# Performance work log

Hardware: AMD Instinct MI355X
Metric: run time of the kernel (lower is better)

## Reference

```python
import jax, jax.numpy as jnp
import numpy as np

H = 384
W = 384
C_X = 64       # channels of x (== out_channels)
C_PTX = 64     # channels of ptx
C_IN = C_X + C_PTX  # Linear in_channels = 128
C_OUT = 64
N_TGT = 120000  # number of target pixels (CSR segments)
DEG = 8         # points per target pixel
N_PTS = N_TGT * DEG


def setup_inputs() -> dict:
    key = jax.random.key(0)
    k1, k2, k3, k4 = jax.random.split(key, 4)
    x = jax.random.normal(k1, (1, C_X, H, W), jnp.float32)
    ptx = jax.random.normal(k2, (N_PTS, C_PTX), jnp.float32)
    # CSR row pointer over points per target pixel (monotone, ends at N_PTS)
    point_key = jnp.arange(N_TGT + 1, dtype=jnp.int32) * DEG
    # unique target-pixel indices into H*W
    pixel_tgt_idx = jnp.arange(N_TGT, dtype=jnp.int32)
    sm_w = jax.random.normal(k3, (C_IN, 1), jnp.float32) * 0.05
    sm_b = jnp.zeros((1,), jnp.float32)
    fo_w = jax.random.normal(k4, (C_IN, C_OUT), jnp.float32) * 0.05
    fo_b = jnp.zeros((C_OUT,), jnp.float32)
    return {"x": x, "ptx": ptx, "sm_w": sm_w, "sm_b": sm_b,
            "fo_w": fo_w, "fo_b": fo_b, "point_key": point_key,
            "pixel_tgt_idx": pixel_tgt_idx, "bs": 1, "height": H, "width": W}


def reference(x, ptx, sm_w, sm_b, fo_w, fo_b, point_key, pixel_tgt_idx, bs, height, width):
    # segment id per point from CSR rowptr (static total length for jit)
    seg = jnp.repeat(jnp.arange(N_TGT, dtype=jnp.int32), jnp.diff(point_key),
                     total_repeat_length=N_PTS)
    # pixel features gathered to target pixels, then CSR-gathered to points
    feat_px = x.transpose(0, 2, 3, 1).reshape(height * width, C_X)[pixel_tgt_idx]
    feat = jnp.concatenate([ptx, feat_px[seg]], axis=1)  # [N_PTS, C_IN]
    # _net_forward: identity (base class)
    # segment softmax over points within each pixel group
    logits = feat @ sm_w + sm_b  # [N_PTS, 1]
    m = jax.ops.segment_max(logits, seg, num_segments=N_TGT)
    e = jnp.exp(logits - m[seg])
    s = jax.ops.segment_sum(e, seg, num_segments=N_TGT)
    weight = e / (s[seg] + 1e-16)
    # feat_out projection replaces ptx
    ptx_out = feat @ fo_w + fo_b  # [N_PTS, C_OUT]
    agg = jax.ops.segment_sum(weight * ptx_out, seg, num_segments=N_TGT)  # [N_TGT, C_OUT]
    # list_to_map: scatter aggregated features back to image grid + mask
    flat = jnp.zeros((height * width, C_OUT), x.dtype).at[pixel_tgt_idx].set(agg)
    mask = jnp.zeros((height * width, 1), x.dtype).at[pixel_tgt_idx].set(1.0)
    fmap = flat.reshape(1, height, width, C_OUT).transpose(0, 3, 1, 2)
    mmap = mask.reshape(1, height, width, 1).transpose(0, 3, 1, 2)
    x_out = jnp.where(mmap > 0, fmap, x)
    return x_out, ptx_out
```

## Files before the change

### kernel.cpp

```cpp
#include <hip/hip_runtime.h>
#include <hip/hip_bf16.h>
#include <math.h>

typedef __attribute__((ext_vector_type(8))) short short8v;
typedef __attribute__((ext_vector_type(4))) short short4v;
typedef __attribute__((ext_vector_type(4))) float float4v;

#define TB 64

__device__ __forceinline__ short f2bf(float f) {
    __hip_bfloat16 h = __float2bfloat16(f);
    short s; __builtin_memcpy(&s, &h, sizeof(short));
    return s;
}
__device__ __forceinline__ float bf2f(short u) {
    unsigned int x = ((unsigned int)(unsigned short)u) << 16;
    float f; __builtin_memcpy(&f, &x, sizeof(float));
    return f;
}
__device__ __forceinline__ float4v mfma_bf16(short8v a, short8v b, float4v c) {
    return __builtin_amdgcn_mfma_f32_16x16x32_bf16(a, b, c, 0, 0, 0);
}

__device__ __forceinline__ int WTI(int row, int col) {
    return row * 72 + (col ^ (((row >> 2) & 7) << 3));
}

__global__ __launch_bounds__(256)
void mask_set_kernel(const int* __restrict__ idx, unsigned char* __restrict__ mask, int n) {
    int i = blockIdx.x * blockDim.x + threadIdx.x;
    if (i < n) mask[idx[i]] = 1;
}

__global__ __launch_bounds__(256)
void copy_masked_kernel(const float4* __restrict__ x, float4* __restrict__ out,
                        const unsigned int* __restrict__ mask4, int q4n) {
    int q = blockIdx.x * blockDim.x + threadIdx.x;
    if (q >= q4n) return;
    if (mask4[q] == 0x01010101u) return;
    size_t idx = (size_t)blockIdx.y * q4n + q;
    out[idx] = x[idx];
}

__global__ __launch_bounds__(256)
void copy_x_kernel(const float4* __restrict__ x, float4* __restrict__ out, int n4) {
    int i = blockIdx.x * blockDim.x + threadIdx.x;
    if (i < n4) out[i] = x[i];
}

__global__ __launch_bounds__(256, 4)
void fused_kernel(const float* __restrict__ x,
                  const float* __restrict__ ptx,
                  const float* __restrict__ sm_w,
                  const float* __restrict__ fo_w,
                  const float* __restrict__ fo_b,
                  const int* __restrict__ point_key,
                  const int* __restrict__ pixel_tgt_idx,
                  float* __restrict__ xout,
                  float* __restrict__ ptx_out,
                  int n_tgt, int n_pts, int hw)
{
    __shared__ __align__(16) char sraw[27648];
    unsigned short (*fpx)[72]   = (unsigned short (*)[72])sraw;
    unsigned short* wTf         = (unsigned short*)(sraw + 9216);
    unsigned short (*q_lds)[72] = (unsigned short (*)[72])sraw;
    float (*agg)[68]            = (float (*)[68])(sraw + 9216);
    __shared__ int pix_s[TB], r0_s[TB], deg_s[TB];

    const int tid  = threadIdx.x;
    const int lane = tid & 63;
    const int w    = tid >> 6;
    const int lo16 = lane & 15;
    const int g    = lane >> 4;
    const int t0   = blockIdx.x * TB;
    const int tw0  = w * 16;

    float4 wv[8];
    {
        const float4* fw4 = (const float4*)fo_w;
        #pragma unroll
        for (int i = 0; i < 8; ++i) wv[i] = fw4[i * 256 + tid];
    }
    float4 fb40 = *(const float4*)&fo_b[ 0 + g * 4];
    float4 fb41 = *(const float4*)&fo_b[16 + g * 4];
    float4 fb42 = *(const float4*)&fo_b[32 + g * 4];
    float4 fb43 = *(const float4*)&fo_b[48 + g * 4];
    if (tid < TB) {
        int t = t0 + tid;
        bool v = t < n_tgt;
        int r0 = v ? point_key[t] : 0;
        int d  = v ? (point_key[t + 1] - r0) : 0;
        pix_s[tid] = v ? pixel_tgt_idx[t] : 0;
        r0_s[tid]  = r0;
        deg_s[tid] = d > 8 ? 8 : d;
    }

    #pragma unroll
    for (int i = 0; i < 8; ++i) {
        int flat = (i * 256 + tid) * 4;
        int k = flat >> 6, c = flat & 63;
        int wrow0 = (k & 64) + c;
        int col = k & 63;
        wTf[WTI(wrow0 + 0, col)] = (unsigned short)f2bf(wv[i].x);
        wTf[WTI(wrow0 + 1, col)] = (unsigned short)f2bf(wv[i].y);
        wTf[WTI(wrow0 + 2, col)] = (unsigned short)f2bf(wv[i].z);
        wTf[WTI(wrow0 + 3, col)] = (unsigned short)f2bf(wv[i].w);
    }
    __syncthreads();

    int pgm[8];
    #pragma unroll
    for (int mt = 0; mt < 8; ++mt) {
        int tlA = tw0 + mt * 2 + (lo16 >> 3);
        int pg  = r0_s[tlA] + (lo16 & 7);
        pgm[mt] = pg < n_pts ? pg : n_pts - 1;
    }

    {
        const int tgt = tid >> 2, q4 = tid & 3;
        const int pix = pix_s[tgt];
        const float* xp = x + (size_t)(q4 * 16) * hw + pix;
        #pragma unroll
        for (int hhalf = 0; hhalf < 2; ++hhalf) {
            short8v pk;
            #pragma unroll
            for (int j = 0; j < 8; ++j)
                pk[j] = f2bf(xp[(size_t)(hhalf * 8 + j) * hw]);
            *(short8v*)&fpx[tgt][q4 * 16 + hhalf * 8] = pk;
        }
    }

    short8v b1[5][2];
    #pragma unroll
    for (int ct = 0; ct < 4; ++ct)
        #pragma unroll
        for (int kh = 0; kh < 2; ++kh)
            b1[ct][kh] = *(const short8v*)&wTf[WTI(ct * 16 + lo16, kh * 32 + g * 8)];
    #pragma unroll
    for (int kh = 0; kh < 2; ++kh) {
        short8v bb;
        #pragma unroll
        for (int j = 0; j < 8; ++j)
            bb[j] = f2bf(sm_w[kh * 32 + g * 8 + j]);
        b1[4][kh] = bb;
    }

    float4 lb0, lb1, lb2, lb3;
    {
        const float* prow = ptx + (size_t)pgm[0] * 64 + g * 8;
        lb0 = *(const float4*)(prow);
        lb1 = *(const float4*)(prow + 4);
        lb2 = *(const float4*)(prow + 32);
        lb3 = *(const float4*)(prow + 36);
    }
    __syncthreads();

    float4v qv4[4];
    {
        short8v a20 = *(const short8v*)&fpx[tw0 + lo16][g * 8];
        short8v a21 = *(const short8v*)&fpx[tw0 + lo16][32 + g * 8];
        #pragma unroll
        for (int ct = 0; ct < 4; ++ct) {
            short8v b20 = *(const short8v*)&wTf[WTI(64 + ct * 16 + lo16, g * 8)];
            short8v b21 = *(const short8v*)&wTf[WTI(64 + ct * 16 + lo16, 32 + g * 8)];
            float4v z = {0.f, 0.f, 0.f, 0.f};
            z = mfma_bf16(b20, a20, z);
            qv4[ct] = mfma_bf16(b21, a21, z);
        }
    }
    __syncthreads();
    {
        short4v q0, q1, q2, q3;
        q0[0] = f2bf(qv4[0][0] + fb40.x); q0[1] = f2bf(qv4[0][1] + fb40.y);
        q0[2] = f2bf(qv4[0][2] + fb40.z); q0[3] = f2bf(qv4[0][3] + fb40.w);
        q1[0] = f2bf(qv4[1][0] + fb41.x); q1[1] = f2bf(qv4[1][1] + fb41.y);
        q1[2] = f2bf(qv4[1][2] + fb41.z); q1[3] = f2bf(qv4[1][3] + fb41.w);
        q2[0] = f2bf(qv4[2][0] + fb42.x); q2[1] = f2bf(qv4[2][1] + fb42.y);
        q2[2] = f2bf(qv4[2][2] + fb42.z); q2[3] = f2bf(qv4[2][3] + fb42.w);
        q3[0] = f2bf(qv4[3][0] + fb43.x); q3[1] = f2bf(qv4[3][1] + fb43.y);
        q3[2] = f2bf(qv4[3][2] + fb43.z); q3[3] = f2bf(qv4[3][3] + fb43.w);
        *(short4v*)&q_lds[tw0 + lo16][ 0 + g * 4] = q0;
        *(short4v*)&q_lds[tw0 + lo16][16 + g * 4] = q1;
        *(short4v*)&q_lds[tw0 + lo16][32 + g * 4] = q2;
        *(short4v*)&q_lds[tw0 + lo16][48 + g * 4] = q3;
    }

#define EPIL_CT(CT, CREG)                                                      \
    {                                                                          \
        const int colb = (CT) * 16 + g * 4;                                    \
        const short4v qb = *(const short4v*)&q_lds[tE][colb];                  \
        float4v po;                                                            \
        po[0] = CREG[0] + bf2f(qb[0]); po[1] = CREG[1] + bf2f(qb[1]);          \
        po[2] = CREG[2] + bf2f(qb[2]); po[3] = CREG[3] + bf2f(qb[3]);          \
        if (val)                                                               \
            *(float4v*)&ptx_out[(size_t)(r0E + pE) * 64 + colb] = po;          \
        float s0 = po[0] * wn, s1 = po[1] * wn, s2 = po[2] * wn, s3 = po[3] * wn; \
        s0 += __shfl_xor(s0, 1); s1 += __shfl_xor(s1, 1);                      \
        s2 += __shfl_xor(s2, 1); s3 += __shfl_xor(s3, 1);                      \
        s0 += __shfl_xor(s0, 2); s1 += __shfl_xor(s1, 2);                      \
        s2 += __shfl_xor(s2, 2); s3 += __shfl_xor(s3, 2);                      \
        s0 += __shfl_xor(s0, 4); s1 += __shfl_xor(s1, 4);                      \
        s2 += __shfl_xor(s2, 4); s3 += __shfl_xor(s3, 4);                      \
        if (pE == 0) {                                                         \
            float4v ag; ag[0] = s0; ag[1] = s1; ag[2] = s2; ag[3] = s3;        \
            *(float4v*)&agg[tE][colb] = ag;                                    \
        }                                                                      \
    }

    #pragma unroll
    for (int mt = 0; mt < 8; ++mt) {
        short8v a0, a1;
        a0[0] = f2bf(lb0.x); a0[1] = f2bf(lb0.y); a0[2] = f2bf(lb0.z); a0[3] = f2bf(lb0.w);
        a0[4] = f2bf(lb1.x); a0[5] = f2bf(lb1.y); a0[6] = f2bf(lb1.z); a0[7] = f2bf(lb1.w);
        a1[0] = f2bf(lb2.x); a1[1] = f2bf(lb2.y); a1[2] = f2bf(lb2.z); a1[3] = f2bf(lb2.w);
        a1[4] = f2bf(lb3.x); a1[5] = f2bf(lb3.y); a1[6] = f2bf(lb3.z); a1[7] = f2bf(lb3.w);

        if (mt < 7) {
            const float* prow = ptx + (size_t)pgm[mt + 1] * 64 + g * 8;
            lb0 = *(const float4*)(prow);
            lb1 = *(const float4*)(prow + 4);
            lb2 = *(const float4*)(prow + 32);
            lb3 = *(const float4*)(prow + 36);
        }

        float4v z = {0.f, 0.f, 0.f, 0.f};
        float4v cc0 = mfma_bf16(b1[0][1], a1, mfma_bf16(b1[0][0], a0, z));
        float4v cc1 = mfma_bf16(b1[1][1], a1, mfma_bf16(b1[1][0], a0, z));
        float4v cc2 = mfma_bf16(b1[2][1], a1, mfma_bf16(b1[2][0], a0, z));
        float4v cc3 = mfma_bf16(b1[3][1], a1, mfma_bf16(b1[3][0], a0, z));
        float4v cc4 = mfma_bf16(b1[4][1], a1, mfma_bf16(b1[4][0], a0, z));

        const int tE   = tw0 + mt * 2 + (lo16 >> 3);
        const int degE = deg_s[tE];
        const int r0E  = r0_s[tE];
        const int pE   = lo16 & 7;
        const bool val = (pE < degE);

        float lg = val ? cc4[0] : -3.4e38f;
        float mx = lg;
        mx = fmaxf(mx, __shfl_xor(mx, 1));
        mx = fmaxf(mx, __shfl_xor(mx, 2));
        mx = fmaxf(mx, __shfl_xor(mx, 4));
        float e = val ? __expf(lg - mx) : 0.0f;
        float sm = e;
        sm += __shfl_xor(sm, 1);
        sm += __shfl_xor(sm, 2);
        sm += __shfl_xor(sm, 4);
        const float wn = e / (sm + 1e-16f);

        EPIL_CT(0, cc0)
        EPIL_CT(1, cc1)
        EPIL_CT(2, cc2)
        EPIL_CT(3, cc3)
    }
#undef EPIL_CT
    __syncthreads();

    {
        const int tgt = tid >> 2, q4 = tid & 3;
        if (t0 + tgt < n_tgt) {
            const int pix = pix_s[tgt];
            float* xp = xout + (size_t)(q4 * 16) * hw + pix;
            #pragma unroll
            for (int u = 0; u < 4; ++u) {
                float4 v = *(const float4*)&agg[tgt][q4 * 16 + u * 4];
                xp[(size_t)(u * 4 + 0) * hw] = v.x;
                xp[(size_t)(u * 4 + 1) * hw] = v.y;
                xp[(size_t)(u * 4 + 2) * hw] = v.z;
                xp[(size_t)(u * 4 + 3) * hw] = v.w;
            }
        }
    }
}

extern "C" void kernel_launch(void* const* d_in, const int* in_sizes, int n_in,
                              void* d_out, int out_size, void* d_ws, size_t ws_size,
                              hipStream_t stream) {
    const float* x             = (const float*)d_in[0];
    const float* ptx           = (const float*)d_in[1];
    const float* sm_w          = (const float*)d_in[2];
    const float* fo_w          = (const float*)d_in[4];
    const float* fo_b          = (const float*)d_in[5];
    const int*   point_key     = (const int*)d_in[6];
    const int*   pixel_tgt_idx = (const int*)d_in[7];

    const int x_elems = in_sizes[0];
    const int hw      = x_elems / 64;
    const int n_tgt   = in_sizes[7];
    const int n_pts   = in_sizes[1] / 64;

    float* xout    = (float*)d_out;
    float* ptx_out = xout + (size_t)x_elems;

    if (ws_size >= (size_t)hw && (hw & 3) == 0) {
        hipMemsetAsync(d_ws, 0, (size_t)hw, stream);
        mask_set_kernel<<<(n_tgt + 255) / 256, 256, 0, stream>>>(
            pixel_tgt_idx, (unsigned char*)d_ws, n_tgt);
        const int q4n = hw / 4;
        dim3 cgrid((q4n + 255) / 256, 64);
        copy_masked_kernel<<<cgrid, 256, 0, stream>>>(
            (const float4*)x, (float4*)xout, (const unsigned int*)d_ws, q4n);
    } else {
        const int n4 = x_elems / 4;
        copy_x_kernel<<<(n4 + 255) / 256, 256, 0, stream>>>(
            (const float4*)x, (float4*)xout, n4);
    }

    const int blocks = (n_tgt + TB - 1) / TB;
    fused_kernel<<<blocks, 256, 0, stream>>>(
        x, ptx, sm_w, fo_w, fo_b, point_key, pixel_tgt_idx,
        xout, ptx_out, n_tgt, n_pts, hw);
}
```

Measured before the change: 139.4 us.

## Precompute bf16 weight fragments in a prep kernel and drop block barriers

```diff
diff --git a/kernel.cpp b/kernel.cpp
--- a/kernel.cpp
+++ b/kernel.cpp
@@ -22,37 +22,41 @@
     return __builtin_amdgcn_mfma_f32_16x16x32_bf16(a, b, c, 0, 0, 0);
 }
 
-__device__ __forceinline__ int WTI(int row, int col) {
-    return row * 72 + (col ^ (((row >> 2) & 7) << 3));
-}
-
-__global__ __launch_bounds__(256)
-void mask_set_kernel(const int* __restrict__ idx, unsigned char* __restrict__ mask, int n) {
-    int i = blockIdx.x * blockDim.x + threadIdx.x;
-    if (i < n) mask[idx[i]] = 1;
-}
-
-__global__ __launch_bounds__(256)
-void copy_masked_kernel(const float4* __restrict__ x, float4* __restrict__ out,
-                        const unsigned int* __restrict__ mask4, int q4n) {
-    int q = blockIdx.x * blockDim.x + threadIdx.x;
-    if (q >= q4n) return;
-    if (mask4[q] == 0x01010101u) return;
-    size_t idx = (size_t)blockIdx.y * q4n + q;
-    out[idx] = x[idx];
-}
-
 __global__ __launch_bounds__(256)
 void copy_x_kernel(const float4* __restrict__ x, float4* __restrict__ out, int n4) {
     int i = blockIdx.x * blockDim.x + threadIdx.x;
     if (i < n4) out[i] = x[i];
 }
 
+__global__ __launch_bounds__(256)
+void prep_w_kernel(const float* __restrict__ fo_w, const float* __restrict__ sm_w,
+                   unsigned short* __restrict__ ws) {
+    int t = blockIdx.x * 256 + threadIdx.x;
+    if (t >= 18 * 64) return;
+    const int frag = t >> 6, lane = t & 63;
+    const int lo16 = lane & 15, g = lane >> 4;
+    short8v v;
+    if (frag < 16) {
+        const int isB2 = frag >> 3, f = frag & 7;
+        const int ct = f >> 1, kh = f & 1;
+        const int kbase = isB2 * 64 + kh * 32 + g * 8;
+        const int col = ct * 16 + lo16;
+        #pragma unroll
+        for (int j = 0; j < 8; ++j)
+            v[j] = f2bf(fo_w[(size_t)(kbase + j) * 64 + col]);
+    } else {
+        const int kh = frag & 1;
+        #pragma unroll
+        for (int j = 0; j < 8; ++j)
+            v[j] = f2bf(sm_w[kh * 32 + g * 8 + j]);
+    }
+    *(short8v*)&ws[(size_t)t * 8] = v;
+}
+
 __global__ __launch_bounds__(256, 4)
 void fused_kernel(const float* __restrict__ x,
                   const float* __restrict__ ptx,
-                  const float* __restrict__ sm_w,
-                  const float* __restrict__ fo_w,
+                  const unsigned short* __restrict__ ws,
                   const float* __restrict__ fo_b,
                   const int* __restrict__ point_key,
                   const int* __restrict__ pixel_tgt_idx,
@@ -60,12 +64,11 @@
                   float* __restrict__ ptx_out,
                   int n_tgt, int n_pts, int hw)
 {
-    __shared__ __align__(16) char sraw[27648];
+    __shared__ __align__(16) unsigned short sraw[64 * 72];
+    __shared__ __align__(16) unsigned short agg_b[64][72];
+    __shared__ int pix_s[TB], r0_s[TB], deg_s[TB];
     unsigned short (*fpx)[72]   = (unsigned short (*)[72])sraw;
-    unsigned short* wTf         = (unsigned short*)(sraw + 9216);
     unsigned short (*q_lds)[72] = (unsigned short (*)[72])sraw;
-    float (*agg)[68]            = (float (*)[68])(sraw + 9216);
-    __shared__ int pix_s[TB], r0_s[TB], deg_s[TB];
 
     const int tid  = threadIdx.x;
     const int lane = tid & 63;
@@ -75,16 +78,6 @@
     const int t0   = blockIdx.x * TB;
     const int tw0  = w * 16;
 
-    float4 wv[8];
-    {
-        const float4* fw4 = (const float4*)fo_w;
-        #pragma unroll
-        for (int i = 0; i < 8; ++i) wv[i] = fw4[i * 256 + tid];
-    }
-    float4 fb40 = *(const float4*)&fo_b[ 0 + g * 4];
-    float4 fb41 = *(const float4*)&fo_b[16 + g * 4];
-    float4 fb42 = *(const float4*)&fo_b[32 + g * 4];
-    float4 fb43 = *(const float4*)&fo_b[48 + g * 4];
     if (tid < TB) {
         int t = t0 + tid;
         bool v = t < n_tgt;
@@ -94,18 +87,6 @@
         r0_s[tid]  = r0;
         deg_s[tid] = d > 8 ? 8 : d;
     }
-
-    #pragma unroll
-    for (int i = 0; i < 8; ++i) {
-        int flat = (i * 256 + tid) * 4;
-        int k = flat >> 6, c = flat & 63;
-        int wrow0 = (k & 64) + c;
-        int col = k & 63;
-        wTf[WTI(wrow0 + 0, col)] = (unsigned short)f2bf(wv[i].x);
-        wTf[WTI(wrow0 + 1, col)] = (unsigned short)f2bf(wv[i].y);
-        wTf[WTI(wrow0 + 2, col)] = (unsigned short)f2bf(wv[i].z);
-        wTf[WTI(wrow0 + 3, col)] = (unsigned short)f2bf(wv[i].w);
-    }
     __syncthreads();
 
     int pgm[8];
@@ -135,15 +116,10 @@
     for (int ct = 0; ct < 4; ++ct)
         #pragma unroll
         for (int kh = 0; kh < 2; ++kh)
-            b1[ct][kh] = *(const short8v*)&wTf[WTI(ct * 16 + lo16, kh * 32 + g * 8)];
-    #pragma unroll
-    for (int kh = 0; kh < 2; ++kh) {
-        short8v bb;
-        #pragma unroll
-        for (int j = 0; j < 8; ++j)
-            bb[j] = f2bf(sm_w[kh * 32 + g * 8 + j]);
-        b1[4][kh] = bb;
-    }
+            b1[ct][kh] = *(const short8v*)&ws[(size_t)((ct * 2 + kh) * 64 + lane) * 8];
+    #pragma unroll
+    for (int kh = 0; kh < 2; ++kh)
+        b1[4][kh] = *(const short8v*)&ws[(size_t)((16 + kh) * 64 + lane) * 8];
 
     float4 lb0, lb1, lb2, lb3;
     {
@@ -153,7 +129,6 @@
         lb2 = *(const float4*)(prow + 32);
         lb3 = *(const float4*)(prow + 36);
     }
-    __syncthreads();
 
     float4v qv4[4];
     {
@@ -161,15 +136,18 @@
         short8v a21 = *(const short8v*)&fpx[tw0 + lo16][32 + g * 8];
         #pragma unroll
         for (int ct = 0; ct < 4; ++ct) {
-            short8v b20 = *(const short8v*)&wTf[WTI(64 + ct * 16 + lo16, g * 8)];
-            short8v b21 = *(const short8v*)&wTf[WTI(64 + ct * 16 + lo16, 32 + g * 8)];
+            short8v b20 = *(const short8v*)&ws[(size_t)((8 + ct * 2 + 0) * 64 + lane) * 8];
+            short8v b21 = *(const short8v*)&ws[(size_t)((8 + ct * 2 + 1) * 64 + lane) * 8];
             float4v z = {0.f, 0.f, 0.f, 0.f};
             z = mfma_bf16(b20, a20, z);
             qv4[ct] = mfma_bf16(b21, a21, z);
         }
     }
-    __syncthreads();
-    {
+    {
+        float4 fb40 = *(const float4*)&fo_b[ 0 + g * 4];
+        float4 fb41 = *(const float4*)&fo_b[16 + g * 4];
+        float4 fb42 = *(const float4*)&fo_b[32 + g * 4];
+        float4 fb43 = *(const float4*)&fo_b[48 + g * 4];
         short4v q0, q1, q2, q3;
         q0[0] = f2bf(qv4[0][0] + fb40.x); q0[1] = f2bf(qv4[0][1] + fb40.y);
         q0[2] = f2bf(qv4[0][2] + fb40.z); q0[3] = f2bf(qv4[0][3] + fb40.w);
@@ -202,8 +180,10 @@
         s0 += __shfl_xor(s0, 4); s1 += __shfl_xor(s1, 4);                      \
         s2 += __shfl_xor(s2, 4); s3 += __shfl_xor(s3, 4);                      \
         if (pE == 0) {                                                         \
-            float4v ag; ag[0] = s0; ag[1] = s1; ag[2] = s2; ag[3] = s3;        \
-            *(float4v*)&agg[tE][colb] = ag;                                    \
+            short4v ag;                                                        \
+            ag[0] = f2bf(s0); ag[1] = f2bf(s1);                                \
+            ag[2] = f2bf(s2); ag[3] = f2bf(s3);                                \
+            *(short4v*)&agg_b[tE][colb] = ag;                                  \
         }                                                                      \
     }
 
@@ -254,7 +234,6 @@
         EPIL_CT(3, cc3)
     }
 #undef EPIL_CT
-    __syncthreads();
 
     {
         const int tgt = tid >> 2, q4 = tid & 3;
@@ -263,11 +242,11 @@
             float* xp = xout + (size_t)(q4 * 16) * hw + pix;
             #pragma unroll
             for (int u = 0; u < 4; ++u) {
-                float4 v = *(const float4*)&agg[tgt][q4 * 16 + u * 4];
-                xp[(size_t)(u * 4 + 0) * hw] = v.x;
-                xp[(size_t)(u * 4 + 1) * hw] = v.y;
-                xp[(size_t)(u * 4 + 2) * hw] = v.z;
-                xp[(size_t)(u * 4 + 3) * hw] = v.w;
+                short4v v = *(const short4v*)&agg_b[tgt][q4 * 16 + u * 4];
+                xp[(size_t)(u * 4 + 0) * hw] = bf2f(v[0]);
+                xp[(size_t)(u * 4 + 1) * hw] = bf2f(v[1]);
+                xp[(size_t)(u * 4 + 2) * hw] = bf2f(v[2]);
+                xp[(size_t)(u * 4 + 3) * hw] = bf2f(v[3]);
             }
         }
     }
@@ -292,22 +271,14 @@
     float* xout    = (float*)d_out;
     float* ptx_out = xout + (size_t)x_elems;
 
-    if (ws_size >= (size_t)hw && (hw & 3) == 0) {
-        hipMemsetAsync(d_ws, 0, (size_t)hw, stream);
-        mask_set_kernel<<<(n_tgt + 255) / 256, 256, 0, stream>>>(
-            pixel_tgt_idx, (unsigned char*)d_ws, n_tgt);
-        const int q4n = hw / 4;
-        dim3 cgrid((q4n + 255) / 256, 64);
-        copy_masked_kernel<<<cgrid, 256, 0, stream>>>(
-            (const float4*)x, (float4*)xout, (const unsigned int*)d_ws, q4n);
-    } else {
-        const int n4 = x_elems / 4;
-        copy_x_kernel<<<(n4 + 255) / 256, 256, 0, stream>>>(
-            (const float4*)x, (float4*)xout, n4);
-    }
+    const int n4 = x_elems / 4;
+    copy_x_kernel<<<(n4 + 255) / 256, 256, 0, stream>>>(
+        (const float4*)x, (float4*)xout, n4);
+
+    prep_w_kernel<<<5, 256, 0, stream>>>(fo_w, sm_w, (unsigned short*)d_ws);
 
     const int blocks = (n_tgt + TB - 1) / TB;
     fused_kernel<<<blocks, 256, 0, stream>>>(
-        x, ptx, sm_w, fo_w, fo_b, point_key, pixel_tgt_idx,
+        x, ptx, (const unsigned short*)d_ws, fo_b, point_key, pixel_tgt_idx,
         xout, ptx_out, n_tgt, n_pts, hw);
 }
```

After: 140.0 us. No clear change (+0.4%).
